# Kernel optimization log

Hardware: AMD Instinct MI355X
Metric: run time of the kernel (lower is better)

The kernel has to match this reference:

```python
import jax, jax.numpy as jnp
import numpy as np

N, T, V, F, K, FO = 8, 64, 200, 64, 3, 64


def setup_inputs() -> dict:
    key = jax.random.key(0)
    k1, k2, k3, k4 = jax.random.split(key, 4)
    x = jax.random.normal(k1, (N, T, V, F), dtype=jnp.float32)
    Att = jax.random.uniform(k2, (N, V, V), dtype=jnp.float32)
    S = jax.random.uniform(k3, (N, T, V, V), dtype=jnp.float32)
    Theta = jax.random.normal(k4, (K, F, FO), dtype=jnp.float32) * 0.1
    return {"x": x, "Att": Att, "S": S, "Theta": Theta}


def reference(x, Att, S, Theta):
    # x: (N,T,V,F); Att: (N,V,V); S: (N,T,V,V); Theta: (K,F,FO)
    n, t, v, f = x.shape
    k_order = Theta.shape[0]
    # symmetrize S by elementwise min with its transpose (last two dims)
    S = jnp.minimum(S, jnp.swapaxes(S, -1, -2))
    eye = jnp.eye(v, dtype=x.dtype)
    # D = diag_embed(sum(A, dim=1)) per timestep -> column sums over axis 2
    d = jnp.sum(S, axis=2)                      # (N,T,V)
    L = d[..., :, None] * eye - S               # (N,T,V,V), D - A
    L_t = L - eye                               # tilde-L
    # Chebyshev recursion (elementwise, matching original code exactly)
    polys = [jnp.broadcast_to(eye, (1, 1, v, v)), L_t][:k_order]
    for _ in range(2, k_order):
        polys.append(2.0 * L_t * polys[-1] - polys[-2])
    Att_b = Att[:, None]                        # (N,1,V,V), broadcast over T
    out = jnp.zeros((n, t, v, Theta.shape[-1]), dtype=x.dtype)
    for kk in range(k_order):
        T_k_att = polys[kk] * Att_b             # (N,T,V,V) (broadcast for k=0)
        # rhs = T_k_att^T @ x : sum over vertex u
        rhs = jnp.einsum('...uv,...uf->...vf', T_k_att, x)  # (N,T,V,F)
        out = out + rhs @ Theta[kk]             # (N,T,V,FO)
    return jax.nn.relu(out)
```

## Files before the change

### kernel.cpp

```cpp
#include <hip/hip_runtime.h>

namespace {

typedef __attribute__((ext_vector_type(8)))  short          short8;
typedef __attribute__((ext_vector_type(8)))  unsigned short u16x8;
typedef __attribute__((ext_vector_type(4)))  unsigned short u16x4;
typedef __attribute__((ext_vector_type(4)))  float          f32x4;

constexpr int V   = 200;
constexpr int VP  = 208;
constexpr int UP  = 224;
constexpr int F   = 64;
constexpr int FO  = 64;
constexpr int NT  = 512;

constexpr size_t WS_SMIN  = 0;
constexpr size_t WS_D     = 47710208;
constexpr size_t WS_SDIAG = 48136192;
constexpr size_t WS_ATTT  = 48562176;
constexpr size_t WS_ADIAG = 50167808;
constexpr size_t WS_THT   = 50174976;

__device__ __forceinline__ unsigned short f2bf(float x) {
    union { float f; unsigned u; } c; c.f = x;
    unsigned r = c.u + 0x7FFF + ((c.u >> 16) & 1);
    return (unsigned short)(r >> 16);
}
__device__ __forceinline__ float bf2f(unsigned short h) {
    union { unsigned u; float f; } c; c.u = ((unsigned)h) << 16;
    return c.f;
}

__global__ __launch_bounds__(256)
void prep_smin(const float* __restrict__ S,
               unsigned short* __restrict__ smin,
               float* __restrict__ d_ws,
               float* __restrict__ sdiag)
{
    __shared__ float As[32][33];
    __shared__ float Bs[32][33];
    __shared__ float Ms[32][33];

    const int b   = blockIdx.x;
    const int tid = threadIdx.x;
    int rem = blockIdx.y, ti = 0;
    while (rem >= 7 - ti) { rem -= 7 - ti; ++ti; }
    const int tj = ti + rem;
    const bool diag = (ti == tj);

    const float* __restrict__ Sp = S + (size_t)b * (V * V);
    unsigned short* __restrict__ smp = smin + (size_t)b * (VP * UP);

    const int r  = tid >> 3;
    const int cg = tid & 7;
    const int c0 = 4 * cg;

    {
        const int gr = 32 * ti + r, gc = 32 * tj + c0;
        float4 a = make_float4(0.f, 0.f, 0.f, 0.f);
        if (gr < V && gc < V) a = *(const float4*)&Sp[gr * V + gc];
        As[r][c0 + 0] = a.x; As[r][c0 + 1] = a.y; As[r][c0 + 2] = a.z; As[r][c0 + 3] = a.w;
        if (!diag) {
            const int hr = 32 * tj + r, hc = 32 * ti + c0;
            float4 bb = make_float4(0.f, 0.f, 0.f, 0.f);
            if (hr < V && hc < V) bb = *(const float4*)&Sp[hr * V + hc];
            Bs[r][c0 + 0] = bb.x; Bs[r][c0 + 1] = bb.y; Bs[r][c0 + 2] = bb.z; Bs[r][c0 + 3] = bb.w;
        }
    }
    __syncthreads();

    float m[4], rs = 0.f;
    #pragma unroll
    for (int e = 0; e < 4; ++e) {
        const int c = c0 + e;
        const float tw = diag ? As[c][r] : Bs[c][r];
        m[e] = fminf(As[r][c], tw);
        Ms[r][c] = m[e];
        rs += m[e];
    }
    rs += __shfl_xor(rs, 1); rs += __shfl_xor(rs, 2); rs += __shfl_xor(rs, 4);
    if (cg == 0 && 32 * ti + r < V)
        atomicAdd(&d_ws[b * VP + 32 * ti + r], rs);
    if (diag && cg == 0 && 32 * ti + r < V)
        sdiag[b * VP + 32 * ti + r] = As[r][r];
    __syncthreads();

    if (!diag) {
        float ts = 0.f;
        #pragma unroll
        for (int e = 0; e < 4; ++e) ts += Ms[c0 + e][r];
        ts += __shfl_xor(ts, 1); ts += __shfl_xor(ts, 2); ts += __shfl_xor(ts, 4);
        if (cg == 0 && 32 * tj + r < V)
            atomicAdd(&d_ws[b * VP + 32 * tj + r], ts);
    }

    {
        const int vr = 32 * ti + r;
        if (vr < VP) {
            u16x4 w;
            #pragma unroll
            for (int e = 0; e < 4; ++e) w[e] = f2bf(m[e]);
            *(u16x4*)&smp[vr * UP + 32 * tj + c0] = w;
        }
        if (!diag) {
            const int vr2 = 32 * tj + r;
            if (vr2 < VP) {
                u16x4 w2;
                #pragma unroll
                for (int e = 0; e < 4; ++e) w2[e] = f2bf(Ms[c0 + e][r]);
                *(u16x4*)&smp[vr2 * UP + 32 * ti + c0] = w2;
            }
        }
    }
}

__global__ __launch_bounds__(256)
void prep_att(const float* __restrict__ Att,
              float* __restrict__ attT,
              float* __restrict__ adiag)
{
    __shared__ float T[32][33];
    const int n  = blockIdx.x;
    const int ut = blockIdx.y / 7, vt = blockIdx.y % 7;
    const int tid = threadIdx.x;

    for (int idx = tid; idx < 1024; idx += 256) {
        const int rr = idx >> 5, cc = idx & 31;
        const int u = 32 * ut + rr, v = 32 * vt + cc;
        T[rr][cc] = (u < V && v < V) ? Att[(size_t)n * (V * V) + u * V + v] : 0.f;
    }
    __syncthreads();
    for (int idx = tid; idx < 1024; idx += 256) {
        const int r2 = idx >> 5, c2 = idx & 31;
        attT[(size_t)n * (UP * UP) + (32 * vt + r2) * UP + 32 * ut + c2] = T[c2][r2];
    }
    if (ut == vt && tid < 32)
        adiag[n * UP + 32 * vt + tid] = T[tid][tid];
}

__global__ __launch_bounds__(256)
void prep_theta(const float* __restrict__ Theta,
                unsigned short* __restrict__ thT)
{
    __shared__ float T[64][65];
    const int k = blockIdx.x, tid = threadIdx.x;
    for (int idx = tid; idx < 4096; idx += 256)
        T[idx >> 6][idx & 63] = Theta[k * 4096 + idx];
    __syncthreads();
    for (int idx = tid; idx < 4096; idx += 256) {
        const int fo = idx >> 6, f = idx & 63;
        thT[k * 4096 + fo * 64 + f] = f2bf(T[f][fo]);
    }
}

constexpr int XS_S = 68;
constexpr int A_S  = 40;
constexpr int YS_S = 72;

__global__ __launch_bounds__(256, 2)
void cheb_main(const float* __restrict__ x,
               const unsigned short* __restrict__ thT,
               const unsigned short* __restrict__ smin,
               const float* __restrict__ d_ws,
               const float* __restrict__ sdiag,
               const float* __restrict__ attT,
               const float* __restrict__ adiag,
               float* __restrict__ out)
{
    __shared__ __align__(16) char smem[65408];
    unsigned short* xs  = (unsigned short*)smem;
    unsigned short* A1  = (unsigned short*)(smem + 30464);
    unsigned short* A2  = (unsigned short*)(smem + 47104);
    unsigned short* ys  = (unsigned short*)smem;
    unsigned short* ThS = (unsigned short*)(smem + 30464);
    float*        cbuf  = (float*)(smem + 63744);
    float*       adbuf  = (float*)(smem + 64576);

    const int tid = threadIdx.x;
    const int b   = blockIdx.x;
    const int n   = b >> 6;
    const float* __restrict__ xp = x + (size_t)b * (V * F);
    const unsigned short* __restrict__ sm = smin + (size_t)b * (VP * UP);
    const float* __restrict__ atp = attT + (size_t)n * (UP * UP);
    float* __restrict__ op = out + (size_t)b * (V * FO);

    for (int idx = tid; idx < UP * 16; idx += 256) {
        const int u = idx >> 4, fg = idx & 15;
        u16x4 w; w[0] = 0; w[1] = 0; w[2] = 0; w[3] = 0;
        if (u < V) {
            const float4 v = *(const float4*)&xp[u * F + 4 * fg];
            w[0] = f2bf(v.x); w[1] = f2bf(v.y); w[2] = f2bf(v.z); w[3] = f2bf(v.w);
        }
        *(u16x4*)&xs[u * XS_S + 4 * fg] = w;
    }
    if (tid < VP) {
        cbuf[tid]  = d_ws[b * VP + tid] - 1.0f - sdiag[b * VP + tid];
        adbuf[tid] = adiag[n * UP + tid];
    }

    const int wave = tid >> 6, lane = tid & 63;
    const int q = lane >> 4, ln = lane & 15;
    const int myBase = (wave == 0) ? 0 : (4 + 3 * (wave - 1));
    const int myCnt  = (wave == 0) ? 4 : 3;

    f32x4 acc1[4][4], acc2[4][4];
    #pragma unroll
    for (int i = 0; i < 4; ++i)
        #pragma unroll
        for (int j = 0; j < 4; ++j) {
            acc1[i][j] = (f32x4)0.f; acc2[i][j] = (f32x4)0.f;
        }

    u16x8 pf_s[4]; float4 pf_a0[4], pf_a1[4];
    auto load_chunks = [&](int kt) {
        const int u0 = 32 * kt;
        #pragma unroll
        for (int c = 0; c < 4; ++c) {
            const int idx = tid + 256 * c;
            if (idx < VP * 4) {
                const int v = idx >> 2, ch = idx & 3;
                const int u8 = u0 + 8 * ch;
                pf_s[c]  = *(const u16x8*)&sm[v * UP + u8];
                pf_a0[c] = *(const float4*)&atp[v * UP + u8];
                pf_a1[c] = *(const float4*)&atp[v * UP + u8 + 4];
            }
        }
    };
    load_chunks(0);

    for (int kt = 0; kt < 7; ++kt) {
        const int u0 = 32 * kt;
        __syncthreads();
        #pragma unroll
        for (int c = 0; c < 4; ++c) {
            const int idx = tid + 256 * c;
            if (idx < VP * 4) {
                const int v = idx >> 2, ch = idx & 3;
                const int u8 = u0 + 8 * ch;
                const u16x8 s8 = pf_s[c];
                const float att[8] = {pf_a0[c].x, pf_a0[c].y, pf_a0[c].z, pf_a0[c].w,
                                      pf_a1[c].x, pf_a1[c].y, pf_a1[c].z, pf_a1[c].w};
                u16x8 w1, w2;
                #pragma unroll
                for (int jj = 0; jj < 8; ++jj) {
                    const float m = bf2f(s8[jj]);
                    if (u8 + jj == v) { w1[jj] = 0; w2[jj] = 0; }
                    else {
                        w1[jj] = f2bf(-m * att[jj]);
                        w2[jj] = f2bf(2.0f * m * m * att[jj]);
                    }
                }
                *(u16x8*)&A1[v * A_S + 8 * ch] = w1;
                *(u16x8*)&A2[v * A_S + 8 * ch] = w2;
            }
        }
        if (kt < 6) load_chunks(kt + 1);
        __syncthreads();
        short8 bfr[4];
        #pragma unroll
        for (int ft = 0; ft < 4; ++ft)
            #pragma unroll
            for (int j = 0; j < 8; ++j)
                bfr[ft][j] = (short)xs[(u0 + 8 * q + j) * XS_S + 16 * ft + ln];
        #pragma unroll
        for (int vi = 0; vi < 4; ++vi) {
            if (vi < myCnt) {
                const int row = (myBase + vi) * 16 + ln;
                const short8 af1 = *(const short8*)&A1[row * A_S + 8 * q];
                const short8 af2 = *(const short8*)&A2[row * A_S + 8 * q];
                #pragma unroll
                for (int ft = 0; ft < 4; ++ft) {
                    acc1[vi][ft] = __builtin_amdgcn_mfma_f32_16x16x32_bf16(af1, bfr[ft], acc1[vi][ft], 0, 0, 0);
                    acc2[vi][ft] = __builtin_amdgcn_mfma_f32_16x16x32_bf16(af2, bfr[ft], acc2[vi][ft], 0, 0, 0);
                }
            }
        }
    }

    f32x4 ot[4][4];
    #pragma unroll
    for (int i = 0; i < 4; ++i)
        #pragma unroll
        for (int j = 0; j < 4; ++j) ot[i][j] = (f32x4)0.f;

    #pragma unroll
    for (int pass = 0; pass < 3; ++pass) {
        const int k = (pass == 0) ? 1 : (pass == 1) ? 2 : 0;
        __syncthreads();

        if (k == 0) {
            for (int idx = tid; idx < VP * 16; idx += 256) {
                const int v = idx >> 4, fg = idx & 15;
                u16x4 w; w[0] = 0; w[1] = 0; w[2] = 0; w[3] = 0;
                if (v < V) {
                    const float av = adbuf[v];
                    const float4 xv = *(const float4*)&xp[v * F + 4 * fg];
                    w[0] = f2bf(av * xv.x); w[1] = f2bf(av * xv.y);
                    w[2] = f2bf(av * xv.z); w[3] = f2bf(av * xv.w);
                }
                *(u16x4*)&ys[v * YS_S + 4 * fg] = w;
            }
        } else {
            #pragma unroll
            for (int vi = 0; vi < 4; ++vi) {
                if (vi < myCnt) {
                    const int vt = myBase + vi;
                    #pragma unroll
                    for (int ft = 0; ft < 4; ++ft) {
                        const f32x4 a = (k == 1) ? acc1[vi][ft] : acc2[vi][ft];
                        #pragma unroll
                        for (int reg = 0; reg < 4; ++reg) {
                            const int v = vt * 16 + 4 * q + reg;
                            float val = 0.f;
                            if (v < V) {
                                const float cc = cbuf[v];
                                const float dc = ((k == 1) ? cc : (2.0f * cc * cc - 1.0f)) * adbuf[v];
                                val = a[reg] + dc * xp[v * F + 16 * ft + ln];
                            }
                            ys[v * YS_S + 16 * ft + ln] = f2bf(val);
                        }
                    }
                }
            }
        }
        for (int idx = tid; idx < 64 * 8; idx += 256) {
            const int fo = idx >> 3, ch = idx & 7;
            *(u16x8*)&ThS[fo * YS_S + 8 * ch] =
                *(const u16x8*)&thT[k * 4096 + fo * 64 + 8 * ch];
        }
        __syncthreads();
        #pragma unroll
        for (int vi = 0; vi < 4; ++vi) {
            if (vi < myCnt) {
                const int vrow = (myBase + vi) * 16 + ln;
                #pragma unroll
                for (int ks = 0; ks < 2; ++ks) {
                    const short8 af = *(const short8*)&ys[vrow * YS_S + 32 * ks + 8 * q];
                    #pragma unroll
                    for (int fot = 0; fot < 4; ++fot) {
                        const short8 bf = *(const short8*)&ThS[(16 * fot + ln) * YS_S + 32 * ks + 8 * q];
                        ot[vi][fot] = __builtin_amdgcn_mfma_f32_16x16x32_bf16(af, bf, ot[vi][fot], 0, 0, 0);
                    }
                }
            }
        }
    }

    #pragma unroll
    for (int vi = 0; vi < 4; ++vi) {
        if (vi < myCnt) {
            const int vt = myBase + vi;
            #pragma unroll
            for (int fot = 0; fot < 4; ++fot) {
                #pragma unroll
                for (int reg = 0; reg < 4; ++reg) {
                    const int v = vt * 16 + 4 * q + reg;
                    if (v < V)
                        op[v * FO + 16 * fot + ln] = fmaxf(ot[vi][fot][reg], 0.f);
                }
            }
        }
    }
}

}

extern "C" void kernel_launch(void* const* d_in, const int* in_sizes, int n_in,
                              void* d_out, int out_size, void* d_ws, size_t ws_size,
                              hipStream_t stream) {
    const float* x     = (const float*)d_in[0];
    const float* Att   = (const float*)d_in[1];
    const float* S     = (const float*)d_in[2];
    const float* Theta = (const float*)d_in[3];
    float* out         = (float*)d_out;

    char* ws = (char*)d_ws;
    unsigned short* smin = (unsigned short*)(ws + WS_SMIN);
    float* d_sum = (float*)(ws + WS_D);
    float* sdiag = (float*)(ws + WS_SDIAG);
    float* attT  = (float*)(ws + WS_ATTT);
    float* adiag = (float*)(ws + WS_ADIAG);
    unsigned short* thT = (unsigned short*)(ws + WS_THT);

    hipMemsetAsync(d_sum, 0, (size_t)NT * VP * sizeof(float), stream);

    hipLaunchKernelGGL(prep_smin,  dim3(NT, 28), dim3(256), 0, stream, S, smin, d_sum, sdiag);
    hipLaunchKernelGGL(prep_att,   dim3(8, 49),  dim3(256), 0, stream, Att, attT, adiag);
    hipLaunchKernelGGL(prep_theta, dim3(3),      dim3(256), 0, stream, Theta, thT);
    hipLaunchKernelGGL(cheb_main,  dim3(NT),     dim3(256), 0, stream,
                       x, thT, smin, d_sum, sdiag, attT, adiag, out);
}
```

Before: 239.1 us.

## Precompute B1/B2 operand matrices in prep and split main kernel over vertex halves

The prep kernel now fuses the Att multiply and the Chebyshev scaling into the S-min pass, writing the two bf16 operand matrices straight to workspace. That removes the transposed-Att buffer and the per-tile elementwise build in the main kernel. The main kernel is split over two halves of the output vertex rows, which doubles the grid, cuts accumulator registers and LDS, and raises the occupancy hint to 3. x is stored transposed in LDS so the B fragment becomes one vector load. The cost is roughly twice the bf16 workspace traffic from writing two matrices, and each half-block redundantly loads and converts all of x.

```diff
diff --git a/kernel.cpp b/kernel.cpp
--- a/kernel.cpp
+++ b/kernel.cpp
@@ -14,12 +14,12 @@
 constexpr int FO  = 64;
 constexpr int NT  = 512;
 
-constexpr size_t WS_SMIN  = 0;
-constexpr size_t WS_D     = 47710208;
-constexpr size_t WS_SDIAG = 48136192;
-constexpr size_t WS_ATTT  = 48562176;
-constexpr size_t WS_ADIAG = 50167808;
-constexpr size_t WS_THT   = 50174976;
+constexpr size_t WS_B1    = 0;
+constexpr size_t WS_B2    = 47710208;
+constexpr size_t WS_D     = 95420416;
+constexpr size_t WS_SDIAG = 95846400;
+constexpr size_t WS_ADIAG = 96272384;
+constexpr size_t WS_THT   = 96279040;
 
 __device__ __forceinline__ unsigned short f2bf(float x) {
     union { float f; unsigned u; } c; c.f = x;
@@ -32,24 +32,31 @@
 }
 
 __global__ __launch_bounds__(256)
-void prep_smin(const float* __restrict__ S,
-               unsigned short* __restrict__ smin,
-               float* __restrict__ d_ws,
-               float* __restrict__ sdiag)
+void prep_B(const float* __restrict__ S,
+            const float* __restrict__ Att,
+            unsigned short* __restrict__ B1w,
+            unsigned short* __restrict__ B2w,
+            float* __restrict__ d_ws,
+            float* __restrict__ sdiag)
 {
     __shared__ float As[32][33];
     __shared__ float Bs[32][33];
     __shared__ float Ms[32][33];
+    __shared__ float Aa[32][33];
+    __shared__ float Ab[32][33];
 
     const int b   = blockIdx.x;
+    const int n   = b >> 6;
     const int tid = threadIdx.x;
     int rem = blockIdx.y, ti = 0;
     while (rem >= 7 - ti) { rem -= 7 - ti; ++ti; }
     const int tj = ti + rem;
     const bool diag = (ti == tj);
 
-    const float* __restrict__ Sp = S + (size_t)b * (V * V);
-    unsigned short* __restrict__ smp = smin + (size_t)b * (VP * UP);
+    const float* __restrict__ Sp = S   + (size_t)b * (V * V);
+    const float* __restrict__ Ap = Att + (size_t)n * (V * V);
+    unsigned short* __restrict__ b1p = B1w + (size_t)b * (VP * UP);
+    unsigned short* __restrict__ b2p = B2w + (size_t)b * (VP * UP);
 
     const int r  = tid >> 3;
     const int cg = tid & 7;
@@ -58,13 +65,23 @@
     {
         const int gr = 32 * ti + r, gc = 32 * tj + c0;
         float4 a = make_float4(0.f, 0.f, 0.f, 0.f);
-        if (gr < V && gc < V) a = *(const float4*)&Sp[gr * V + gc];
-        As[r][c0 + 0] = a.x; As[r][c0 + 1] = a.y; As[r][c0 + 2] = a.z; As[r][c0 + 3] = a.w;
+        float4 t = make_float4(0.f, 0.f, 0.f, 0.f);
+        if (gr < V && gc < V) {
+            a = *(const float4*)&Sp[gr * V + gc];
+            t = *(const float4*)&Ap[gr * V + gc];
+        }
+        As[r][c0+0]=a.x; As[r][c0+1]=a.y; As[r][c0+2]=a.z; As[r][c0+3]=a.w;
+        Aa[r][c0+0]=t.x; Aa[r][c0+1]=t.y; Aa[r][c0+2]=t.z; Aa[r][c0+3]=t.w;
         if (!diag) {
             const int hr = 32 * tj + r, hc = 32 * ti + c0;
             float4 bb = make_float4(0.f, 0.f, 0.f, 0.f);
-            if (hr < V && hc < V) bb = *(const float4*)&Sp[hr * V + hc];
-            Bs[r][c0 + 0] = bb.x; Bs[r][c0 + 1] = bb.y; Bs[r][c0 + 2] = bb.z; Bs[r][c0 + 3] = bb.w;
+            float4 tb = make_float4(0.f, 0.f, 0.f, 0.f);
+            if (hr < V && hc < V) {
+                bb = *(const float4*)&Sp[hr * V + hc];
+                tb = *(const float4*)&Ap[hr * V + hc];
+            }
+            Bs[r][c0+0]=bb.x; Bs[r][c0+1]=bb.y; Bs[r][c0+2]=bb.z; Bs[r][c0+3]=bb.w;
+            Ab[r][c0+0]=tb.x; Ab[r][c0+1]=tb.y; Ab[r][c0+2]=tb.z; Ab[r][c0+3]=tb.w;
         }
     }
     __syncthreads();
@@ -97,132 +114,142 @@
     {
         const int vr = 32 * ti + r;
         if (vr < VP) {
-            u16x4 w;
+            u16x4 w1, w2;
             #pragma unroll
-            for (int e = 0; e < 4; ++e) w[e] = f2bf(m[e]);
-            *(u16x4*)&smp[vr * UP + 32 * tj + c0] = w;
-        }
-        if (!diag) {
-            const int vr2 = 32 * tj + r;
-            if (vr2 < VP) {
-                u16x4 w2;
-                #pragma unroll
-                for (int e = 0; e < 4; ++e) w2[e] = f2bf(Ms[c0 + e][r]);
-                *(u16x4*)&smp[vr2 * UP + 32 * ti + c0] = w2;
-            }
+            for (int e = 0; e < 4; ++e) {
+                const int c = c0 + e;
+                const float att = diag ? Aa[c][r] : Ab[c][r];
+                const float mm  = Ms[r][c];
+                const bool  dg  = diag && (c == r);
+                w1[e] = dg ? (unsigned short)0 : f2bf(-mm * att);
+                w2[e] = dg ? (unsigned short)0 : f2bf(2.0f * mm * mm * att);
+            }
+            *(u16x4*)&b1p[vr * UP + 32 * tj + c0] = w1;
+            *(u16x4*)&b2p[vr * UP + 32 * tj + c0] = w2;
+        }
+    }
+    if (!diag) {
+        const int vr = 32 * tj + r;
+        if (vr < VP) {
+            u16x4 w1, w2;
+            #pragma unroll
+            for (int e = 0; e < 4; ++e) {
+                const int c = c0 + e;
+                const float att = Aa[c][r];
+                const float mm  = Ms[c][r];
+                w1[e] = f2bf(-mm * att);
+                w2[e] = f2bf(2.0f * mm * mm * att);
+            }
+            *(u16x4*)&b1p[vr * UP + 32 * ti + c0] = w1;
+            *(u16x4*)&b2p[vr * UP + 32 * ti + c0] = w2;
         }
     }
 }
 
 __global__ __launch_bounds__(256)
-void prep_att(const float* __restrict__ Att,
-              float* __restrict__ attT,
-              float* __restrict__ adiag)
+void prep_small(const float* __restrict__ Theta,
+                const float* __restrict__ Att,
+                unsigned short* __restrict__ thT,
+                float* __restrict__ adiag)
 {
-    __shared__ float T[32][33];
-    const int n  = blockIdx.x;
-    const int ut = blockIdx.y / 7, vt = blockIdx.y % 7;
-    const int tid = threadIdx.x;
-
-    for (int idx = tid; idx < 1024; idx += 256) {
-        const int rr = idx >> 5, cc = idx & 31;
-        const int u = 32 * ut + rr, v = 32 * vt + cc;
-        T[rr][cc] = (u < V && v < V) ? Att[(size_t)n * (V * V) + u * V + v] : 0.f;
-    }
-    __syncthreads();
-    for (int idx = tid; idx < 1024; idx += 256) {
-        const int r2 = idx >> 5, c2 = idx & 31;
-        attT[(size_t)n * (UP * UP) + (32 * vt + r2) * UP + 32 * ut + c2] = T[c2][r2];
-    }
-    if (ut == vt && tid < 32)
-        adiag[n * UP + 32 * vt + tid] = T[tid][tid];
-}
-
-__global__ __launch_bounds__(256)
-void prep_theta(const float* __restrict__ Theta,
-                unsigned short* __restrict__ thT)
-{
-    __shared__ float T[64][65];
-    const int k = blockIdx.x, tid = threadIdx.x;
-    for (int idx = tid; idx < 4096; idx += 256)
-        T[idx >> 6][idx & 63] = Theta[k * 4096 + idx];
-    __syncthreads();
-    for (int idx = tid; idx < 4096; idx += 256) {
-        const int fo = idx >> 6, f = idx & 63;
-        thT[k * 4096 + fo * 64 + f] = f2bf(T[f][fo]);
-    }
-}
-
-constexpr int XS_S = 68;
+    const int blk = blockIdx.x, tid = threadIdx.x;
+    if (blk < 3) {
+        __shared__ float T[64][65];
+        for (int idx = tid; idx < 4096; idx += 256)
+            T[idx >> 6][idx & 63] = Theta[blk * 4096 + idx];
+        __syncthreads();
+        for (int idx = tid; idx < 4096; idx += 256) {
+            const int fo = idx >> 6, f = idx & 63;
+            thT[blk * 4096 + fo * 64 + f] = f2bf(T[f][fo]);
+        }
+    } else {
+        for (int idx = tid; idx < 8 * VP; idx += 256) {
+            const int nn = idx / VP, v = idx % VP;
+            adiag[idx] = (v < V) ? Att[(size_t)nn * (V * V) + v * V + v] : 0.f;
+        }
+    }
+}
+
+constexpr int XT_S = 232;
 constexpr int A_S  = 40;
 constexpr int YS_S = 72;
 
-__global__ __launch_bounds__(256, 2)
+constexpr int OFF_XST = 0;
+constexpr int OFF_B1  = 29696;
+constexpr int OFF_B2  = 38912;
+constexpr int OFF_CB  = 48128;
+constexpr int OFF_AD  = 48576;
+constexpr int SMEM_SZ = 49024;
+
+__global__ __launch_bounds__(256, 3)
 void cheb_main(const float* __restrict__ x,
                const unsigned short* __restrict__ thT,
-               const unsigned short* __restrict__ smin,
+               const unsigned short* __restrict__ B1w,
+               const unsigned short* __restrict__ B2w,
                const float* __restrict__ d_ws,
                const float* __restrict__ sdiag,
-               const float* __restrict__ attT,
                const float* __restrict__ adiag,
                float* __restrict__ out)
 {
-    __shared__ __align__(16) char smem[65408];
-    unsigned short* xs  = (unsigned short*)smem;
-    unsigned short* A1  = (unsigned short*)(smem + 30464);
-    unsigned short* A2  = (unsigned short*)(smem + 47104);
-    unsigned short* ys  = (unsigned short*)smem;
-    unsigned short* ThS = (unsigned short*)(smem + 30464);
-    float*        cbuf  = (float*)(smem + 63744);
-    float*       adbuf  = (float*)(smem + 64576);
+    __shared__ __align__(16) char smem[SMEM_SZ];
+    unsigned short* xsT  = (unsigned short*)(smem + OFF_XST);
+    unsigned short* B1s  = (unsigned short*)(smem + OFF_B1);
+    unsigned short* B2s  = (unsigned short*)(smem + OFF_B2);
+    unsigned short* ys   = (unsigned short*)(smem + OFF_XST);
+    unsigned short* ThS  = (unsigned short*)(smem + OFF_B1);
+    float*          cbuf = (float*)(smem + OFF_CB);
+    float*         adbuf = (float*)(smem + OFF_AD);
 
     const int tid = threadIdx.x;
     const int b   = blockIdx.x;
+    const int hv  = blockIdx.y;
     const int n   = b >> 6;
+    const int hvb   = 112 * hv;
+    const int nrows = hv ? 96 : 112;
+
     const float* __restrict__ xp = x + (size_t)b * (V * F);
-    const unsigned short* __restrict__ sm = smin + (size_t)b * (VP * UP);
-    const float* __restrict__ atp = attT + (size_t)n * (UP * UP);
+    const unsigned short* __restrict__ b1p = B1w + (size_t)b * (VP * UP);
+    const unsigned short* __restrict__ b2p = B2w + (size_t)b * (VP * UP);
     float* __restrict__ op = out + (size_t)b * (V * FO);
 
     for (int idx = tid; idx < UP * 16; idx += 256) {
         const int u = idx >> 4, fg = idx & 15;
-        u16x4 w; w[0] = 0; w[1] = 0; w[2] = 0; w[3] = 0;
-        if (u < V) {
-            const float4 v = *(const float4*)&xp[u * F + 4 * fg];
-            w[0] = f2bf(v.x); w[1] = f2bf(v.y); w[2] = f2bf(v.z); w[3] = f2bf(v.w);
-        }
-        *(u16x4*)&xs[u * XS_S + 4 * fg] = w;
-    }
-    if (tid < VP) {
-        cbuf[tid]  = d_ws[b * VP + tid] - 1.0f - sdiag[b * VP + tid];
-        adbuf[tid] = adiag[n * UP + tid];
+        float4 v = make_float4(0.f, 0.f, 0.f, 0.f);
+        if (u < V) v = *(const float4*)&xp[u * F + 4 * fg];
+        xsT[(4 * fg + 0) * XT_S + u] = f2bf(v.x);
+        xsT[(4 * fg + 1) * XT_S + u] = f2bf(v.y);
+        xsT[(4 * fg + 2) * XT_S + u] = f2bf(v.z);
+        xsT[(4 * fg + 3) * XT_S + u] = f2bf(v.w);
+    }
+    if (tid < nrows) {
+        const int g = hvb + tid;
+        cbuf[tid]  = d_ws[b * VP + g] - 1.0f - sdiag[b * VP + g];
+        adbuf[tid] = adiag[n * VP + g];
     }
 
     const int wave = tid >> 6, lane = tid & 63;
     const int q = lane >> 4, ln = lane & 15;
-    const int myBase = (wave == 0) ? 0 : (4 + 3 * (wave - 1));
-    const int myCnt  = (wave == 0) ? 4 : 3;
-
-    f32x4 acc1[4][4], acc2[4][4];
+    const int myBase = (hv == 0) ? 2 * wave : ((wave < 2) ? 2 * wave : wave + 2);
+    const int myCnt  = (hv == 0) ? ((wave == 3) ? 1 : 2) : ((wave < 2) ? 2 : 1);
+
+    f32x4 acc1[2][4], acc2[2][4];
     #pragma unroll
-    for (int i = 0; i < 4; ++i)
-        #pragma unroll
-        for (int j = 0; j < 4; ++j) {
-            acc1[i][j] = (f32x4)0.f; acc2[i][j] = (f32x4)0.f;
-        }
-
-    u16x8 pf_s[4]; float4 pf_a0[4], pf_a1[4];
+    for (int i = 0; i < 2; ++i)
+        #pragma unroll
+        for (int j = 0; j < 4; ++j) { acc1[i][j] = (f32x4)0.f; acc2[i][j] = (f32x4)0.f; }
+
+    u16x8 pf1[2], pf2[2];
+    const int nch = nrows * 4;
     auto load_chunks = [&](int kt) {
         const int u0 = 32 * kt;
         #pragma unroll
-        for (int c = 0; c < 4; ++c) {
+        for (int c = 0; c < 2; ++c) {
             const int idx = tid + 256 * c;
-            if (idx < VP * 4) {
-                const int v = idx >> 2, ch = idx & 3;
-                const int u8 = u0 + 8 * ch;
-                pf_s[c]  = *(const u16x8*)&sm[v * UP + u8];
-                pf_a0[c] = *(const float4*)&atp[v * UP + u8];
-                pf_a1[c] = *(const float4*)&atp[v * UP + u8 + 4];
+            if (idx < nch) {
+                const int row = idx >> 2, ch = idx & 3;
+                const size_t off = (size_t)(hvb + row) * UP + u0 + 8 * ch;
+                pf1[c] = *(const u16x8*)&b1p[off];
+                pf2[c] = *(const u16x8*)&b2p[off];
             }
         }
     };
@@ -232,26 +259,12 @@
         const int u0 = 32 * kt;
         __syncthreads();
         #pragma unroll
-        for (int c = 0; c < 4; ++c) {
+        for (int c = 0; c < 2; ++c) {
             const int idx = tid + 256 * c;
-            if (idx < VP * 4) {
-                const int v = idx >> 2, ch = idx & 3;
-                const int u8 = u0 + 8 * ch;
-                const u16x8 s8 = pf_s[c];
-                const float att[8] = {pf_a0[c].x, pf_a0[c].y, pf_a0[c].z, pf_a0[c].w,
-                                      pf_a1[c].x, pf_a1[c].y, pf_a1[c].z, pf_a1[c].w};
-                u16x8 w1, w2;
-                #pragma unroll
-                for (int jj = 0; jj < 8; ++jj) {
-                    const float m = bf2f(s8[jj]);
-                    if (u8 + jj == v) { w1[jj] = 0; w2[jj] = 0; }
-                    else {
-                        w1[jj] = f2bf(-m * att[jj]);
-                        w2[jj] = f2bf(2.0f * m * m * att[jj]);
-                    }
-                }
-                *(u16x8*)&A1[v * A_S + 8 * ch] = w1;
-                *(u16x8*)&A2[v * A_S + 8 * ch] = w2;
+            if (idx < nch) {
+                const int row = idx >> 2, ch = idx & 3;
+                *(u16x8*)&B1s[row * A_S + 8 * ch] = pf1[c];
+                *(u16x8*)&B2s[row * A_S + 8 * ch] = pf2[c];
             }
         }
         if (kt < 6) load_chunks(kt + 1);
@@ -259,15 +272,13 @@
         short8 bfr[4];
         #pragma unroll
         for (int ft = 0; ft < 4; ++ft)
-            #pragma unroll
-            for (int j = 0; j < 8; ++j)
-                bfr[ft][j] = (short)xs[(u0 + 8 * q + j) * XS_S + 16 * ft + ln];
-        #pragma unroll
-        for (int vi = 0; vi < 4; ++vi) {
+            bfr[ft] = *(const short8*)&xsT[(16 * ft + ln) * XT_S + u0 + 8 * q];
+        #pragma unroll
+        for (int vi = 0; vi < 2; ++vi) {
             if (vi < myCnt) {
                 const int row = (myBase + vi) * 16 + ln;
-                const short8 af1 = *(const short8*)&A1[row * A_S + 8 * q];
-                const short8 af2 = *(const short8*)&A2[row * A_S + 8 * q];
+                const short8 af1 = *(const short8*)&B1s[row * A_S + 8 * q];
+                const short8 af2 = *(const short8*)&B2s[row * A_S + 8 * q];
                 #pragma unroll
                 for (int ft = 0; ft < 4; ++ft) {
                     acc1[vi][ft] = __builtin_amdgcn_mfma_f32_16x16x32_bf16(af1, bfr[ft], acc1[vi][ft], 0, 0, 0);
@@ -277,9 +288,9 @@
         }
     }
 
-    f32x4 ot[4][4];
+    f32x4 ot[2][4];
     #pragma unroll
-    for (int i = 0; i < 4; ++i)
+    for (int i = 0; i < 2; ++i)
         #pragma unroll
         for (int j = 0; j < 4; ++j) ot[i][j] = (f32x4)0.f;
 
@@ -289,35 +300,37 @@
         __syncthreads();
 
         if (k == 0) {
-            for (int idx = tid; idx < VP * 16; idx += 256) {
-                const int v = idx >> 4, fg = idx & 15;
+            for (int idx = tid; idx < nrows * 16; idx += 256) {
+                const int vloc = idx >> 4, fg = idx & 15;
+                const int v = hvb + vloc;
                 u16x4 w; w[0] = 0; w[1] = 0; w[2] = 0; w[3] = 0;
                 if (v < V) {
-                    const float av = adbuf[v];
+                    const float av = adbuf[vloc];
                     const float4 xv = *(const float4*)&xp[v * F + 4 * fg];
                     w[0] = f2bf(av * xv.x); w[1] = f2bf(av * xv.y);
                     w[2] = f2bf(av * xv.z); w[3] = f2bf(av * xv.w);
                 }
-                *(u16x4*)&ys[v * YS_S + 4 * fg] = w;
+                *(u16x4*)&ys[vloc * YS_S + 4 * fg] = w;
             }
         } else {
             #pragma unroll
-            for (int vi = 0; vi < 4; ++vi) {
+            for (int vi = 0; vi < 2; ++vi) {
                 if (vi < myCnt) {
-                    const int vt = myBase + vi;
+                    const int row16 = (myBase + vi) * 16;
                     #pragma unroll
                     for (int ft = 0; ft < 4; ++ft) {
                         const f32x4 a = (k == 1) ? acc1[vi][ft] : acc2[vi][ft];
                         #pragma unroll
                         for (int reg = 0; reg < 4; ++reg) {
-                            const int v = vt * 16 + 4 * q + reg;
+                            const int vloc = row16 + 4 * q + reg;
+                            const int v = hvb + vloc;
                             float val = 0.f;
                             if (v < V) {
-                                const float cc = cbuf[v];
-                                const float dc = ((k == 1) ? cc : (2.0f * cc * cc - 1.0f)) * adbuf[v];
+                                const float cc = cbuf[vloc];
+                                const float dc = ((k == 1) ? cc : (2.0f * cc * cc - 1.0f)) * adbuf[vloc];
                                 val = a[reg] + dc * xp[v * F + 16 * ft + ln];
                             }
-                            ys[v * YS_S + 16 * ft + ln] = f2bf(val);
+                            ys[vloc * YS_S + 16 * ft + ln] = f2bf(val);
                         }
                     }
                 }
@@ -330,7 +343,7 @@
         }
         __syncthreads();
         #pragma unroll
-        for (int vi = 0; vi < 4; ++vi) {
+        for (int vi = 0; vi < 2; ++vi) {
             if (vi < myCnt) {
                 const int vrow = (myBase + vi) * 16 + ln;
                 #pragma unroll
@@ -347,14 +360,14 @@
     }
 
     #pragma unroll
-    for (int vi = 0; vi < 4; ++vi) {
+    for (int vi = 0; vi < 2; ++vi) {
         if (vi < myCnt) {
-            const int vt = myBase + vi;
+            const int row16 = (myBase + vi) * 16;
             #pragma unroll
             for (int fot = 0; fot < 4; ++fot) {
                 #pragma unroll
                 for (int reg = 0; reg < 4; ++reg) {
-                    const int v = vt * 16 + 4 * q + reg;
+                    const int v = hvb + row16 + 4 * q + reg;
                     if (v < V)
                         op[v * FO + 16 * fot + ln] = fmaxf(ot[vi][fot][reg], 0.f);
                 }
@@ -375,18 +388,17 @@
     float* out         = (float*)d_out;
 
     char* ws = (char*)d_ws;
-    unsigned short* smin = (unsigned short*)(ws + WS_SMIN);
+    unsigned short* B1w = (unsigned short*)(ws + WS_B1);
+    unsigned short* B2w = (unsigned short*)(ws + WS_B2);
     float* d_sum = (float*)(ws + WS_D);
     float* sdiag = (float*)(ws + WS_SDIAG);
-    float* attT  = (float*)(ws + WS_ATTT);
     float* adiag = (float*)(ws + WS_ADIAG);
     unsigned short* thT = (unsigned short*)(ws + WS_THT);
 
     hipMemsetAsync(d_sum, 0, (size_t)NT * VP * sizeof(float), stream);
 
-    hipLaunchKernelGGL(prep_smin,  dim3(NT, 28), dim3(256), 0, stream, S, smin, d_sum, sdiag);
-    hipLaunchKernelGGL(prep_att,   dim3(8, 49),  dim3(256), 0, stream, Att, attT, adiag);
-    hipLaunchKernelGGL(prep_theta, dim3(3),      dim3(256), 0, stream, Theta, thT);
-    hipLaunchKernelGGL(cheb_main,  dim3(NT),     dim3(256), 0, stream,
-                       x, thT, smin, d_sum, sdiag, attT, adiag, out);
-}
+    hipLaunchKernelGGL(prep_B,     dim3(NT, 28), dim3(256), 0, stream, S, Att, B1w, B2w, d_sum, sdiag);
+    hipLaunchKernelGGL(prep_small, dim3(4),      dim3(256), 0, stream, Theta, Att, thT, adiag);
+    hipLaunchKernelGGL(cheb_main,  dim3(NT, 2),  dim3(256), 0, stream,
+                       x, thT, B1w, B2w, d_sum, sdiag, adiag, out);
+}
```

Result: slower. 254.6 us (+6.5%).
